# Performance work log

Hardware: AMD Instinct MI355X
Metric: run time of the kernel (lower is better)

Reference implementation:

```python
import jax, jax.numpy as jnp
import numpy as np

R, A, K, N = 4096, 101, 32, 4000000
AEC_LOW, AEC_SPAN = 0.0, 1.0
ETA_NEON, ETA_CHILD, ETA_ADULT = 2.0, 1.5, 1.0
SINK_M = 0.5
FEMALE_SHARE = 0.5
THETA_DEV, PHI_REP, THETA_CYC = 1.0, 1.0, 5.0
RATE_ANN, KAPPA = 0.02, 1.0
WA, RA = 15, 65
INHERIT_CONC, INHERIT_FRAC, BIRTH_ENDOW = 1.0, 0.8, 1.0


def setup_inputs() -> dict:
    key = jax.random.key(0)
    ks = jax.random.split(key, 26)
    dt = 1.0 / 365.0
    pop_age = jax.random.uniform(ks[8], (R, A)) * 1e4
    aging_M = jnp.eye(A) * (1.0 - dt) + jnp.eye(A, A, k=1) * dt
    aging_M = aging_M.at[A - 1, A - 1].set(1.0)
    return {
        'aec_r': jax.random.uniform(ks[0], (R,)) * 2.0,
        'gdp_pc_r': jax.random.uniform(ks[1], (R,)) * 5e4 + 1e3,
        'gdp_pc_ema_R': jax.random.uniform(ks[2], (R,)) * 5e4 + 1e3,
        'gdp_pc_baseline_R': jax.random.uniform(ks[3], (R,)) * 5e4 + 1e3,
        'dev_index_R': jax.random.uniform(ks[4], (R,)),
        'sink_use': jax.random.uniform(ks[5], (R,)),
        'sink_cap': jax.random.uniform(ks[6], (R,)) + 0.5,
        'hazard_A_base': jax.random.uniform(ks[7], (A,)) * 0.1 + 0.001,
        'pop_age': pop_age,
        'population': pop_age.sum(axis=1),
        'aging_M': aging_M,
        'asfr_vector': jax.random.uniform(ks[9], (35,)) * 0.2,
        'distance': jax.random.uniform(ks[10], (R, R)) * 100.0 + 1.0,
        'consump_w_age': jax.random.uniform(ks[11], (A,)),
        'participation_w_age': jax.random.uniform(ks[12], (A,)),
        'consump_base_R': jax.random.uniform(ks[13], (R,)) * 1e4 + 1e3,
        'labor_base_R': jax.random.uniform(ks[14], (R,)) * 1e4 + 1e3,
        'greed': jax.random.uniform(ks[15], (N,)) + 0.01,
        'eATP': jax.random.uniform(ks[16], (N,)) * 100.0,
        'eADP': jax.random.uniform(ks[17], (N,)) * 100.0,
        'eAMP': jax.random.uniform(ks[18], (N,)) * 100.0,
        'pool_atp_R': jax.random.uniform(ks[19], (R,)) * 1e6,
        'pool_adp_R': jax.random.uniform(ks[20], (R,)) * 1e6,
        'pool_amp_R': jax.random.uniform(ks[21], (R,)) * 1e6,
        'nbr_idx': jax.random.randint(ks[22], (R, K), 0, R),
        'agent_region': jax.random.randint(ks[23], (N,), 0, R),
    }


def _forward(aec_r, gdp_pc_r, gdp_pc_ema_R, gdp_pc_baseline_R, dev_index_R, sink_use, sink_cap,
             hazard_A_base, pop_age, population, aging_M, asfr_vector, distance, consump_w_age,
             participation_w_age, consump_base_R, labor_base_R, greed, eATP, eADP, eAMP,
             pool_atp_R, pool_adp_R, pool_amp_R, nbr_idx, agent_region):
    eps = 1e-9
    dt = 1.0 / 365.0
    aec_norm = jnp.clip((aec_r - AEC_LOW) / AEC_SPAN, 0.0, 1.0)
    gdp_prev = gdp_pc_ema_R
    gdp_ema = gdp_prev * 0.9 + 0.1 * gdp_pc_r
    g_ratio = jnp.log(jnp.maximum(gdp_ema / (gdp_pc_baseline_R + eps), 1e-6))
    g_term = jnp.clip(0.5 + 0.5 * jnp.tanh(0.5 * g_ratio), 0.0, 1.0)
    util = jnp.clip(sink_use / (sink_cap + eps), 0.0, 1.0)
    H = jnp.clip(0.5 * aec_norm + 0.4 * g_term + 0.1 * (1.0 - util), 0.0, 1.0)
    dev_proxy = jnp.clip(0.5 + 0.5 * jnp.tanh(0.3 * g_ratio), 0.0, 1.0)
    dev = dev_index_R * 0.99 + 0.01 * dev_proxy
    # age-bucketed hazard multipliers: age 0 / ages 1..14 / ages 15+
    ages = jnp.arange(A)[None, :]
    m_neon = jnp.exp(-ETA_NEON * H)[:, None]
    m_child = jnp.exp(-ETA_CHILD * H)[:, None]
    m_adult = jnp.exp(-ETA_ADULT * H)[:, None]
    mult = jnp.where(ages == 0, m_neon, jnp.where(ages < 15, m_child, m_adult))
    haz = jnp.clip(hazard_A_base[None, :] * mult * (1.0 + SINK_M * util[:, None]), 0.0, 5.0)
    S = jnp.exp(-haz * dt)
    survivors = pop_age * S
    pop_after = survivors @ aging_M  # [R, A]
    deaths_R = jnp.maximum(pop_age.sum(1) - survivors.sum(1), 0.0)
    death_frac_R = jnp.clip(deaths_R / (population + eps), 0.0, 0.99)
    # fertility
    female_RF = FEMALE_SHARE * pop_after[:, 15:50]
    surv_u5 = jnp.exp(-haz[:, 0:5].sum(1))
    F_dev = jnp.clip(jnp.exp(-THETA_DEV * dev), 0.5, 1.5)
    F_rep = jnp.clip((0.995 / jnp.maximum(surv_u5, 1e-3)) ** PHI_REP, 0.5, 1.8)
    g_growth = jnp.log(jnp.maximum(gdp_ema + eps, 1e-6)) - jnp.log(jnp.maximum(gdp_prev + eps, 1e-6))
    F_cyc = jnp.clip(jnp.exp(-THETA_CYC * jnp.maximum(-g_growth, 0.0)), 0.6, 1.2)
    F_total = jnp.clip(F_dev * F_rep * F_cyc, 0.4, 1.8)
    births = jnp.maximum((female_RF * asfr_vector[None, :]).sum(1) * F_total * dt, 0.0)
    births_surv = births * jnp.exp(-haz[:, 0] * dt)
    pop_after = pop_after.at[:, 0].add(births_surv)
    # migration gather-scatter over neighbor regions
    a0, a1 = 18, 40
    mobile = pop_after[:, a0:a1]
    attract = 0.6 * (gdp_pc_r / (gdp_pc_baseline_R + eps)) + 0.4 * (0.5 + 0.5 * aec_norm)
    attract = attract / (attract.mean() + eps)
    dist = jnp.take_along_axis(distance, nbr_idx, axis=1)  # [R, K]
    cost = 1.0 + dist / (dist.mean() + eps)
    w = jax.nn.relu(attract[nbr_idx] / cost ** KAPPA)
    w = w / (w.sum(1, keepdims=True) + eps)
    frac_move = min(max(RATE_ANN * dt, 0.0), 0.25)
    out_R = mobile.sum(1) * frac_move
    move = out_R[:, None] * w  # [R, K]
    age_share = mobile / (mobile.sum(1, keepdims=True) + eps)
    pop_after = pop_after.at[:, a0:a1].add(-age_share * move.sum(1, keepdims=True))
    inflow = (age_share[:, None, :] * move[:, :, None]).reshape(R * K, a1 - a0)
    add = jnp.zeros((R, a1 - a0), pop_after.dtype).at[nbr_idx.reshape(-1)].add(inflow)
    pop_after = pop_after.at[:, a0:a1].add(add)
    pop_new = jnp.maximum(pop_after, 0.0)
    population_new = jnp.maximum(pop_new.sum(1), 0.0)
    consump_scale = jnp.clip((pop_new * consump_w_age[None, :]).sum(1) / (consump_base_R + eps), 0.25, 4.0)
    labor_factor = jnp.clip((pop_new * participation_w_age[None, :]).sum(1) / (labor_base_R + eps), 0.2, 1.2)
    work = pop_new[:, WA:RA].sum(1)
    young = pop_new[:, :WA].sum(1)
    old = pop_new[:, RA:].sum(1)
    psr = work / (old + eps)
    dep = (young + old) / (work + eps)
    # agent-level death / inheritance scatters
    dfi = death_frac_R[agent_region]
    w_raw = (greed + 1e-9) ** INHERIT_CONC
    w_sum_r = jax.ops.segment_sum(w_raw, agent_region, num_segments=R)
    w_norm = w_raw / (w_sum_r[agent_region] + eps)

    def settle(wallet, pool):
        removed = wallet * dfi
        removed_pool = jax.ops.segment_sum(removed, agent_region, num_segments=R)
        heir_pool = removed_pool * INHERIT_FRAC
        wallet2 = wallet - removed + w_norm * heir_pool[agent_region]
        return wallet2, pool - (removed_pool - heir_pool)

    eATP2, pool_atp2 = settle(eATP, pool_atp_R)
    eADP2, pool_adp2 = settle(eADP, pool_adp_R)
    eAMP2, pool_amp2 = settle(eAMP, pool_amp_R)
    counts = jax.ops.segment_sum(jnp.ones_like(dfi), agent_region, num_segments=R)
    eATP2 = eATP2 + BIRTH_ENDOW * (births_surv / jnp.maximum(counts, 1.0))[agent_region]
    return (pop_new, population_new, gdp_ema, dev, H, consump_scale, labor_factor, psr, dep,
            eATP2, eADP2, eAMP2, pool_atp2, pool_adp2, pool_amp2)


def reference(aec_r, gdp_pc_r, gdp_pc_ema_R, gdp_pc_baseline_R, dev_index_R, sink_use, sink_cap,
              hazard_A_base, pop_age, population, aging_M, asfr_vector, distance, consump_w_age,
              participation_w_age, consump_base_R, labor_base_R, greed, eATP, eADP, eAMP,
              pool_atp_R, pool_adp_R, pool_amp_R, nbr_idx, agent_region):
    return _forward(aec_r, gdp_pc_r, gdp_pc_ema_R, gdp_pc_baseline_R, dev_index_R, sink_use,
                    sink_cap, hazard_A_base, pop_age, population, aging_M, asfr_vector, distance,
                    consump_w_age, participation_w_age, consump_base_R, labor_base_R, greed,
                    eATP, eADP, eAMP, pool_atp_R, pool_adp_R, pool_amp_R, nbr_idx, agent_region)
```

## Files before the change

kernel.cpp:

```cpp
#include <hip/hip_runtime.h>

#define RR 4096
#define AA 101
#define PAD_W 104
#define KK 32
#define NAG 4000000

#define NCHUNK 32
#define DR 512
#define NRANGE 8
#define EPB (RR * KK / NCHUNK)
#define CH 8
#define NB 512

static constexpr float EPS  = 1e-9f;
static constexpr float DT   = 1.0f / 365.0f;
static constexpr float FRAC_MOVE = 0.02f / 365.0f;

static constexpr float SC13  = 8192.0f;
static constexpr float INV13 = 1.0f / 8192.0f;
static constexpr float SC20  = 1048576.0f;
static constexpr float INV20 = 1.0f / 1048576.0f;
static constexpr float SC18  = 262144.0f;
static constexpr float INV18 = 1.0f / 262144.0f;

#define OUT_POP   0
#define OUT_POPN  413696
#define OUT_GDP   417792
#define OUT_DEV   421888
#define OUT_H     425984
#define OUT_CONS  430080
#define OUT_LAB   434176
#define OUT_PSR   438272
#define OUT_DEP   442368
#define OUT_ATP   446464
#define OUT_ADP   4446464
#define OUT_AMP   8446464
#define OUT_PATP  12446464
#define OUT_PADP  12450560
#define OUT_PAMP  12454656

static __device__ __forceinline__ float clampf(float x, float lo, float hi) {
    return fminf(fmaxf(x, lo), hi);
}
static __device__ __forceinline__ float wred(float x) {
#pragma unroll
    for (int m = 32; m; m >>= 1) x += __shfl_xor(x, m);
    return x;
}

__global__ __launch_bounds__(256) void k_region1(
    const float* __restrict__ aec, const float* __restrict__ gdp_pc,
    const float* __restrict__ gdp_ema_in, const float* __restrict__ gdp_base,
    const float* __restrict__ dev_in, const float* __restrict__ sink_use,
    const float* __restrict__ sink_cap, const float* __restrict__ haz_base,
    const float* __restrict__ pop_age, const float* __restrict__ population,
    const float* __restrict__ aging, const float* __restrict__ asfr,
    const float* __restrict__ distance, const int* __restrict__ nbr,
    float* __restrict__ Wpa, float* __restrict__ Wdfrac, float* __restrict__ Wbsurv,
    float* __restrict__ Wattr, float* __restrict__ Wgdist, float* __restrict__ Wdsum,
    float* __restrict__ O)
{
    int wid = threadIdx.x >> 6, lane = threadIdx.x & 63;
    int r = blockIdx.x * 4 + wid;

    float aec_norm = clampf(aec[r], 0.0f, 1.0f);
    float gprev = gdp_ema_in[r];
    float gema  = gprev * 0.9f + 0.1f * gdp_pc[r];
    float base  = gdp_base[r];
    float g_ratio = logf(fmaxf(gema / (base + EPS), 1e-6f));
    float g_term  = clampf(0.5f + 0.5f * tanhf(0.5f * g_ratio), 0.0f, 1.0f);
    float util = clampf(sink_use[r] / (sink_cap[r] + EPS), 0.0f, 1.0f);
    float H = clampf(0.5f * aec_norm + 0.4f * g_term + 0.1f * (1.0f - util), 0.0f, 1.0f);
    float dev_proxy = clampf(0.5f + 0.5f * tanhf(0.3f * g_ratio), 0.0f, 1.0f);
    float dev = dev_in[r] * 0.99f + 0.01f * dev_proxy;

    float m_neon  = expf(-2.0f * H);
    float m_child = expf(-1.5f * H);
    float m_adult = expf(-1.0f * H);
    float hazmul = 1.0f + 0.5f * util;

    int a0 = lane * 2, a1 = a0 + 1;
    bool v0 = (a0 < AA), v1 = (a1 < AA);

    float p0 = 0.f, p1 = 0.f, hz0 = 0.f, hz1 = 0.f;
    if (v0) {
        p0 = pop_age[r * AA + a0];
        float mult = (a0 == 0) ? m_neon : ((a0 < 15) ? m_child : m_adult);
        hz0 = clampf(haz_base[a0] * mult * hazmul, 0.0f, 5.0f);
    }
    if (v1) {
        p1 = pop_age[r * AA + a1];
        float mult = (a1 < 15) ? m_child : m_adult;
        hz1 = clampf(haz_base[a1] * mult * hazmul, 0.0f, 5.0f);
    }
    float s0 = v0 ? p0 * expf(-hz0 * DT) : 0.f;
    float s1 = v1 ? p1 * expf(-hz1 * DT) : 0.f;
    float sp = __shfl_up(s1, 1);

    float Md0 = 0.f, Md1 = 0.f, Ms0 = 0.f, Ms1 = 0.f;
    if (v0) { Md0 = aging[a0 * AA + a0]; if (a0 > 0) Ms0 = aging[(a0 - 1) * AA + a0]; }
    if (v1) { Md1 = aging[a1 * AA + a1]; Ms1 = aging[(a1 - 1) * AA + a1]; }

    float pa0 = v0 ? ((a0 == 0) ? s0 * Md0 : s0 * Md0 + sp * Ms0) : 0.f;
    float pa1 = v1 ? (s1 * Md1 + s0 * Ms1) : 0.f;

    if (v0 && a0 > 0) Wpa[r * PAD_W + a0] = pa0;
    if (v1)           Wpa[r * PAD_W + a1] = pa1;

    float pop_sum  = wred(p0 + p1);
    float surv_sum = wred(s0 + s1);
    float haz05 = wred(((v0 && a0 < 5) ? hz0 : 0.f) + ((v1 && a1 < 5) ? hz1 : 0.f));
    float bs0 = (a0 >= 15 && a0 < 50) ? 0.5f * pa0 * asfr[a0 - 15] : 0.f;
    float bs1 = (a1 >= 15 && a1 < 50) ? 0.5f * pa1 * asfr[a1 - 15] : 0.f;
    float b_sum = wred(bs0 + bs1);

    float dc = 0.f;
    if (lane < KK) {
        int idx = nbr[r * KK + lane];
        float d = distance[(size_t)r * RR + idx];
        Wgdist[r * KK + lane] = d;
        dc = d;
    }
    float dsum = wred(dc);

    if (lane == 0) {
        O[OUT_GDP + r] = gema;
        O[OUT_DEV + r] = dev;
        O[OUT_H + r]   = H;

        float deaths = fmaxf(pop_sum - surv_sum, 0.0f);
        Wdfrac[r] = clampf(deaths / (population[r] + EPS), 0.0f, 0.99f);

        float surv_u5 = expf(-haz05);
        float F_dev = clampf(expf(-dev), 0.5f, 1.5f);
        float F_rep = clampf(0.995f / fmaxf(surv_u5, 0.001f), 0.5f, 1.8f);
        float g_growth = logf(fmaxf(gema + EPS, 1e-6f)) - logf(fmaxf(gprev + EPS, 1e-6f));
        float F_cyc = clampf(expf(-5.0f * fmaxf(-g_growth, 0.0f)), 0.6f, 1.2f);
        float F_total = clampf(F_dev * F_rep * F_cyc, 0.4f, 1.8f);
        float births = fmaxf(b_sum * F_total * DT, 0.0f);
        float bsurv = births * expf(-hz0 * DT);
        Wbsurv[r] = bsurv;
        Wpa[r * PAD_W + 0] = pa0 + bsurv;

        Wattr[r] = 0.6f * (gdp_pc[r] / (base + EPS)) + 0.4f * (0.5f + 0.5f * aec_norm);
        Wdsum[r] = dsum;
    }
}

__global__ __launch_bounds__(256) void k_migrate_a(
    const int* __restrict__ nbr, const float* __restrict__ Wattr,
    const float* __restrict__ Wgdist, const float* __restrict__ Wdsum,
    float* __restrict__ Wpa, float* __restrict__ Wash, float* __restrict__ Wmove)
{
    __shared__ float sred[8];
    int t = threadIdx.x;
    {
        float a = 0.f, d = 0.f;
        for (int i = t; i < RR; i += 256) { a += Wattr[i]; d += Wdsum[i]; }
        a = wred(a); d = wred(d);
        int w0 = t >> 6;
        if ((t & 63) == 0) { sred[w0] = a; sred[4 + w0] = d; }
    }
    __syncthreads();
    float asum = sred[0] + sred[1] + sred[2] + sred[3];
    float dall = sred[4] + sred[5] + sred[6] + sred[7];
    float inv_am = 1.0f / (asum / (float)RR + EPS);
    float inv_dm = 1.0f / (dall / (float)(RR * KK) + EPS);

    int wid = t >> 6, lane = t & 63;
    int r = blockIdx.x * 4 + wid;

    float mob = 0.f;
    if (lane < 22) mob = Wpa[r * PAD_W + 18 + lane];
    float msum = wred(lane < 22 ? mob : 0.f);

    float w = 0.f;
    if (lane < KK) {
        int idx = nbr[r * KK + lane];
        float an = Wattr[idx] * inv_am;
        float cost = 1.0f + Wgdist[r * KK + lane] * inv_dm;
        w = fmaxf(an / cost, 0.0f);
    }
    float wsum = wred(lane < KK ? w : 0.f);

    float out_R = msum * FRAC_MOVE;
    float invw = 1.0f / (wsum + EPS);
    float move_sum = out_R * wsum * invw;
    float inv_ms = 1.0f / (msum + EPS);

    if (lane < 22) {
        float ash = mob * inv_ms;
        Wash[r * 22 + lane] = ash;
        Wpa[r * PAD_W + 18 + lane] = mob - ash * move_sum;
    }
    if (lane < KK) Wmove[r * KK + lane] = out_R * w * invw;
}

__global__ __launch_bounds__(256) void k_migrate_b(
    const int* __restrict__ nbr, const float* __restrict__ Wash,
    const float* __restrict__ Wmove, float* __restrict__ Smig)
{
    __shared__ unsigned long long h[11 * DR];
    int range = blockIdx.x & (NRANGE - 1);
    int chunk = blockIdx.x >> 3;
    int d0 = range * DR;

    for (int i = threadIdx.x; i < 11 * DR; i += 256) h[i] = 0ull;
    __syncthreads();

    int tend = (chunk + 1) * EPB;
    for (int t = chunk * EPB + threadIdx.x; t < tend; t += 256) {
        int idx = nbr[t];
        if (idx >= d0 && idx < d0 + DR) {
            int rsrc = t >> 5;
            float mv = Wmove[t];
            const float* ash = &Wash[rsrc * 22];
            int dl = idx - d0;
#pragma unroll
            for (int f = 0; f < 11; f++) {
                unsigned long long lo = __float2uint_rn(ash[2 * f] * mv * SC18);
                unsigned long long hi = __float2uint_rn(ash[2 * f + 1] * mv * SC18);
                atomicAdd(&h[f * DR + dl], lo | (hi << 32));
            }
        }
    }
    __syncthreads();

    for (int i = threadIdx.x; i < 11 * DR; i += 256) {
        int f = i / DR, d = i - f * DR;
        unsigned long long v = h[i];
        Smig[(chunk * 22 + 2 * f) * RR + d0 + d]     = (float)(unsigned int)v * INV18;
        Smig[(chunk * 22 + 2 * f + 1) * RR + d0 + d] = (float)(v >> 32) * INV18;
    }
}

__global__ __launch_bounds__(512, 4) void k_hist(
    const int* __restrict__ reg, const float* __restrict__ greed,
    const float* __restrict__ atp, const float* __restrict__ adp,
    const float* __restrict__ amp, float* __restrict__ S)
{
    __shared__ unsigned long long hAB[RR];
    __shared__ unsigned long long hMGC[RR];
    for (int i = threadIdx.x; i < RR; i += 512) { hAB[i] = 0ull; hMGC[i] = 0ull; }
    __syncthreads();

    const int4*   reg4 = (const int4*)reg;
    const float4* g4 = (const float4*)greed;
    const float4* a4 = (const float4*)atp;
    const float4* d4 = (const float4*)adp;
    const float4* m4 = (const float4*)amp;
    const int NQ = NAG / 4;
    const int STRIDE = NB * 512;

    int q0 = blockIdx.x * 512 + threadIdx.x;
    int4 rrv[4]; float4 gv[4], av[4], dv[4], mv[4];
    bool ok[4];
#pragma unroll
    for (int c = 0; c < 4; c++) {
        int q = q0 + c * STRIDE;
        ok[c] = (q < NQ);
        int qq = ok[c] ? q : 0;
        rrv[c] = reg4[qq];
        gv[c] = g4[qq];
        av[c] = a4[qq];
        dv[c] = d4[qq];
        mv[c] = m4[qq];
    }

#pragma unroll
    for (int c = 0; c < 4; c++) {
        if (!ok[c]) continue;
#define DO1(RX, GX, AX, DX, MX) { \
        unsigned long long ai = __float2uint_rn((AX) * SC13); \
        unsigned long long di = __float2uint_rn((DX) * SC13); \
        unsigned long long mi = __float2uint_rn((MX) * SC13); \
        unsigned long long gi = __float2uint_rn(((GX) + 1e-9f) * SC20); \
        atomicAdd(&hAB[RX],  ai | (di << 32)); \
        atomicAdd(&hMGC[RX], mi | (gi << 28) | (1ull << 56)); }
        DO1(rrv[c].x, gv[c].x, av[c].x, dv[c].x, mv[c].x)
        DO1(rrv[c].y, gv[c].y, av[c].y, dv[c].y, mv[c].y)
        DO1(rrv[c].z, gv[c].z, av[c].z, dv[c].z, mv[c].z)
        DO1(rrv[c].w, gv[c].w, av[c].w, dv[c].w, mv[c].w)
#undef DO1
    }
    __syncthreads();

    int b = blockIdx.x;
    for (int i = threadIdx.x; i < RR; i += 512) {
        unsigned long long ab = hAB[i], mgc = hMGC[i];
        S[((size_t)0 * NB + b) * RR + i] = (float)(unsigned int)ab * INV13;
        S[((size_t)1 * NB + b) * RR + i] = (float)(ab >> 32) * INV13;
        S[((size_t)2 * NB + b) * RR + i] = (float)(mgc & 0xFFFFFFFull) * INV13;
        S[((size_t)3 * NB + b) * RR + i] = (float)((mgc >> 28) & 0xFFFFFFFull) * INV20;
        S[((size_t)4 * NB + b) * RR + i] = (float)(mgc >> 56);
    }
}

__global__ __launch_bounds__(256) void k_reduce(
    const float* __restrict__ S, const float* __restrict__ Smig,
    float* __restrict__ T, float* __restrict__ Wadd)
{
    int blk = blockIdx.x;
    if (blk < 640) {
        int tid = blk * 256 + threadIdx.x;
        int r = tid & (RR - 1);
        int c = (tid >> 12) & (CH - 1);
        int s = tid >> 15;
        int bpc = NB >> 3;
        float acc = 0.f;
        for (int b = c * bpc; b < (c + 1) * bpc; b++)
            acc += S[((size_t)s * NB + b) * RR + r];
        T[(s * CH + c) * RR + r] = acc;
    } else {
        int t2 = (blk - 640) * 256 + threadIdx.x;
        int f = t2 >> 12, rr = t2 & (RR - 1);
        float acc = 0.f;
#pragma unroll
        for (int c = 0; c < NCHUNK; c++)
            acc += Smig[(c * 22 + f) * RR + rr];
        Wadd[rr * 24 + f] = acc;
    }
}

__global__ __launch_bounds__(256) void k_fin(
    const float* __restrict__ Wpa, const float* __restrict__ Wadd,
    const float* __restrict__ cw, const float* __restrict__ pw,
    const float* __restrict__ cbase, const float* __restrict__ lbase,
    const float* __restrict__ T,
    const float* __restrict__ Wdfrac, const float* __restrict__ Wbsurv,
    const float* __restrict__ patp, const float* __restrict__ padp,
    const float* __restrict__ pamp,
    float4* __restrict__ P4, float2* __restrict__ P2,
    float* __restrict__ O)
{
    int blk = blockIdx.x;
    if (blk < 1024) {
        int wid = threadIdx.x >> 6, lane = threadIdx.x & 63;
        int r = blk * 4 + wid;
        int a0 = lane * 2, a1 = a0 + 1;
        bool v0 = (a0 < AA), v1 = (a1 < AA);

        float va = 0.f, vb = 0.f;
        if (lane < 51) {
            float2 pp = *(const float2*)&Wpa[r * PAD_W + a0];
            va = pp.x; vb = pp.y;
        }
        if (a0 >= 18 && a0 < 40) {
            float2 ad = *(const float2*)&Wadd[r * 24 + (a0 - 18)];
            va += ad.x; vb += ad.y;
        }
        va = v0 ? fmaxf(va, 0.0f) : 0.f;
        vb = v1 ? fmaxf(vb, 0.0f) : 0.f;
        if (v0) O[OUT_POP + r * AA + a0] = va;
        if (v1) O[OUT_POP + r * AA + a1] = vb;

        float cw0 = v0 ? cw[a0] : 0.f, cw1 = v1 ? cw[a1] : 0.f;
        float pw0 = v0 ? pw[a0] : 0.f, pw1 = v1 ? pw[a1] : 0.f;

        float psum  = wred(va + vb);
        float cdot  = wred(va * cw0 + vb * cw1);
        float ldot  = wred(va * pw0 + vb * pw1);
        float young = wred(((a0 < 15) ? va : 0.f) + ((a1 < 15) ? vb : 0.f));
        float work  = wred(((a0 >= 15 && a0 < 65) ? va : 0.f) + ((a1 >= 15 && a1 < 65) ? vb : 0.f));
        float old   = wred(((a0 >= 65) ? va : 0.f) + ((a1 >= 65) ? vb : 0.f));

        if (lane == 0) {
            O[OUT_POPN + r] = fmaxf(psum, 0.0f);
            O[OUT_CONS + r] = clampf(cdot / (cbase[r] + EPS), 0.25f, 4.0f);
            O[OUT_LAB + r]  = clampf(ldot / (lbase[r] + EPS), 0.2f, 1.2f);
            O[OUT_PSR + r]  = work / (old + EPS);
            O[OUT_DEP + r]  = (young + old) / (work + EPS);
        }
    } else {
        int r = (blk - 1024) * 256 + threadIdx.x;
        if (r >= RR) return;
        float sums[5];
#pragma unroll
        for (int s = 0; s < 5; s++) {
            float acc = 0.f;
#pragma unroll
            for (int c = 0; c < CH; c++)
                acc += T[(s * CH + c) * RR + r];
            sums[s] = acc;
        }
        float dfi = Wdfrac[r];
        float ra = sums[0] * dfi;
        float rd = sums[1] * dfi;
        float rm = sums[2] * dfi;
        O[OUT_PATP + r] = patp[r] - ra * 0.2f;
        O[OUT_PADP + r] = padp[r] - rd * 0.2f;
        O[OUT_PAMP + r] = pamp[r] - rm * 0.2f;
        P4[r] = make_float4(1.0f - dfi, 1.0f / (sums[3] + EPS), ra * 0.8f, rd * 0.8f);
        P2[r] = make_float2(rm * 0.8f, Wbsurv[r] / fmaxf(sums[4], 1.0f));
    }
}

__global__ __launch_bounds__(256) void k_apply(
    const int* __restrict__ reg, const float* __restrict__ greed,
    const float* __restrict__ atp, const float* __restrict__ adp,
    const float* __restrict__ amp,
    const float4* __restrict__ P4, const float2* __restrict__ P2,
    float* __restrict__ O)
{
    int q = blockIdx.x * 256 + threadIdx.x;
    if (q >= NAG / 4) return;
    int4 rr = ((const int4*)reg)[q];
    float4 g = ((const float4*)greed)[q];
    float4 a = ((const float4*)atp)[q];
    float4 d = ((const float4*)adp)[q];
    float4 m = ((const float4*)amp)[q];
    float4 oa, od, om;
#define ONE(c) { float4 t4 = P4[rr.c]; float2 t2 = P2[rr.c]; \
    float wn = (g.c + 1e-9f) * t4.y; \
    oa.c = a.c * t4.x + wn * t4.z + t2.y; \
    od.c = d.c * t4.x + wn * t4.w; \
    om.c = m.c * t4.x + wn * t2.x; }
    ONE(x) ONE(y) ONE(z) ONE(w)
#undef ONE
    ((float4*)(O + OUT_ATP))[q] = oa;
    ((float4*)(O + OUT_ADP))[q] = od;
    ((float4*)(O + OUT_AMP))[q] = om;
}

extern "C" void kernel_launch(void* const* d_in, const int* in_sizes, int n_in,
                              void* d_out, int out_size, void* d_ws, size_t ws_size,
                              hipStream_t stream) {
    const float* aec       = (const float*)d_in[0];
    const float* gdp_pc    = (const float*)d_in[1];
    const float* gdp_ema   = (const float*)d_in[2];
    const float* gdp_base  = (const float*)d_in[3];
    const float* dev_in    = (const float*)d_in[4];
    const float* sink_use  = (const float*)d_in[5];
    const float* sink_cap  = (const float*)d_in[6];
    const float* haz_base  = (const float*)d_in[7];
    const float* pop_age   = (const float*)d_in[8];
    const float* population= (const float*)d_in[9];
    const float* aging     = (const float*)d_in[10];
    const float* asfr      = (const float*)d_in[11];
    const float* distance  = (const float*)d_in[12];
    const float* cw        = (const float*)d_in[13];
    const float* pw        = (const float*)d_in[14];
    const float* cbase     = (const float*)d_in[15];
    const float* lbase     = (const float*)d_in[16];
    const float* greed     = (const float*)d_in[17];
    const float* eATP      = (const float*)d_in[18];
    const float* eADP      = (const float*)d_in[19];
    const float* eAMP      = (const float*)d_in[20];
    const float* patp      = (const float*)d_in[21];
    const float* padp      = (const float*)d_in[22];
    const float* pamp      = (const float*)d_in[23];
    const int*   nbr       = (const int*)d_in[24];
    const int*   reg       = (const int*)d_in[25];

    float* O = (float*)d_out;

    float* W = (float*)d_ws;
    float* Wpa    = W;
    float* Wdfrac = Wpa    + RR * PAD_W;
    float* Wbsurv = Wdfrac + RR;
    float* Wattr  = Wbsurv + RR;
    float* Wdsum  = Wattr  + RR;
    float* Wgdist = Wdsum  + RR;
    float* Wash   = Wgdist + RR * KK;
    float* Wmove  = Wash   + RR * 22;
    float* P4f    = Wmove  + RR * KK;
    float* P2f    = P4f    + RR * 4;
    float* Wadd   = P2f    + RR * 2;
    float* T      = Wadd   + RR * 24;
    float* Smig   = T      + 5 * CH * RR;
    float* S      = Smig   + (size_t)NCHUNK * 22 * RR;

    k_region1<<<RR / 4, 256, 0, stream>>>(
        aec, gdp_pc, gdp_ema, gdp_base, dev_in, sink_use, sink_cap, haz_base,
        pop_age, population, aging, asfr, distance, nbr,
        Wpa, Wdfrac, Wbsurv, Wattr, Wgdist, Wdsum, O);

    k_migrate_a<<<RR / 4, 256, 0, stream>>>(nbr, Wattr, Wgdist, Wdsum, Wpa, Wash, Wmove);

    k_migrate_b<<<NRANGE * NCHUNK, 256, 0, stream>>>(nbr, Wash, Wmove, Smig);

    k_hist<<<NB, 512, 0, stream>>>(reg, greed, eATP, eADP, eAMP, S);

    k_reduce<<<640 + (22 * RR) / 256, 256, 0, stream>>>(S, Smig, T, Wadd);

    k_fin<<<1024 + RR / 256, 256, 0, stream>>>(
        Wpa, Wadd, cw, pw, cbase, lbase, T, Wdfrac, Wbsurv,
        patp, padp, pamp, (float4*)P4f, (float2*)P2f, O);

    k_apply<<<(NAG / 4 + 255) / 256, 256, 0, stream>>>(
        reg, greed, eATP, eADP, eAMP, (const float4*)P4f, (const float2*)P2f, O);
}
```

Measured before the change: 107.7 us.

## Split histogram kernel into two block groups with one shared histogram each

The per-agent histogram kernel now launches twice as many blocks. Half accumulate the packed ATP/ADP sums and the other half accumulate the packed AMP/greed/count sums, so each block needs only one 32 KB shared array. The smaller shared footprint and the higher launch-bounds occupancy hint are meant to raise occupancy and latency hiding. The cost is that the region index array is read twice, and the register-prefetched unrolled loads become a simple strided loop.

```diff
diff --git a/kernel.cpp b/kernel.cpp
--- a/kernel.cpp
+++ b/kernel.cpp
@@ -235,65 +235,66 @@
     }
 }
 
-__global__ __launch_bounds__(512, 4) void k_hist(
+__global__ __launch_bounds__(512, 8) void k_hist(
     const int* __restrict__ reg, const float* __restrict__ greed,
     const float* __restrict__ atp, const float* __restrict__ adp,
     const float* __restrict__ amp, float* __restrict__ S)
 {
-    __shared__ unsigned long long hAB[RR];
-    __shared__ unsigned long long hMGC[RR];
-    for (int i = threadIdx.x; i < RR; i += 512) { hAB[i] = 0ull; hMGC[i] = 0ull; }
+    __shared__ unsigned long long h[RR];
+    for (int i = threadIdx.x; i < RR; i += 512) h[i] = 0ull;
     __syncthreads();
 
-    const int4*   reg4 = (const int4*)reg;
-    const float4* g4 = (const float4*)greed;
-    const float4* a4 = (const float4*)atp;
-    const float4* d4 = (const float4*)adp;
-    const float4* m4 = (const float4*)amp;
+    const int4* reg4 = (const int4*)reg;
     const int NQ = NAG / 4;
     const int STRIDE = NB * 512;
-
-    int q0 = blockIdx.x * 512 + threadIdx.x;
-    int4 rrv[4]; float4 gv[4], av[4], dv[4], mv[4];
-    bool ok[4];
-#pragma unroll
-    for (int c = 0; c < 4; c++) {
-        int q = q0 + c * STRIDE;
-        ok[c] = (q < NQ);
-        int qq = ok[c] ? q : 0;
-        rrv[c] = reg4[qq];
-        gv[c] = g4[qq];
-        av[c] = a4[qq];
-        dv[c] = d4[qq];
-        mv[c] = m4[qq];
-    }
-
-#pragma unroll
-    for (int c = 0; c < 4; c++) {
-        if (!ok[c]) continue;
-#define DO1(RX, GX, AX, DX, MX) { \
-        unsigned long long ai = __float2uint_rn((AX) * SC13); \
-        unsigned long long di = __float2uint_rn((DX) * SC13); \
-        unsigned long long mi = __float2uint_rn((MX) * SC13); \
-        unsigned long long gi = __float2uint_rn(((GX) + 1e-9f) * SC20); \
-        atomicAdd(&hAB[RX],  ai | (di << 32)); \
-        atomicAdd(&hMGC[RX], mi | (gi << 28) | (1ull << 56)); }
-        DO1(rrv[c].x, gv[c].x, av[c].x, dv[c].x, mv[c].x)
-        DO1(rrv[c].y, gv[c].y, av[c].y, dv[c].y, mv[c].y)
-        DO1(rrv[c].z, gv[c].z, av[c].z, dv[c].z, mv[c].z)
-        DO1(rrv[c].w, gv[c].w, av[c].w, dv[c].w, mv[c].w)
+    int bid = blockIdx.x;
+
+    if (bid < NB) {
+        const float4* a4 = (const float4*)atp;
+        const float4* d4 = (const float4*)adp;
+        for (int q = bid * 512 + threadIdx.x; q < NQ; q += STRIDE) {
+            int4 rr = reg4[q];
+            float4 av = a4[q], dv = d4[q];
+#define DO1(RX, AX, DX) { \
+            unsigned long long ai = __float2uint_rn((AX) * SC13); \
+            unsigned long long di = __float2uint_rn((DX) * SC13); \
+            atomicAdd(&h[RX], ai | (di << 32)); }
+            DO1(rr.x, av.x, dv.x)
+            DO1(rr.y, av.y, dv.y)
+            DO1(rr.z, av.z, dv.z)
+            DO1(rr.w, av.w, dv.w)
 #undef DO1
-    }
-    __syncthreads();
-
-    int b = blockIdx.x;
-    for (int i = threadIdx.x; i < RR; i += 512) {
-        unsigned long long ab = hAB[i], mgc = hMGC[i];
-        S[((size_t)0 * NB + b) * RR + i] = (float)(unsigned int)ab * INV13;
-        S[((size_t)1 * NB + b) * RR + i] = (float)(ab >> 32) * INV13;
-        S[((size_t)2 * NB + b) * RR + i] = (float)(mgc & 0xFFFFFFFull) * INV13;
-        S[((size_t)3 * NB + b) * RR + i] = (float)((mgc >> 28) & 0xFFFFFFFull) * INV20;
-        S[((size_t)4 * NB + b) * RR + i] = (float)(mgc >> 56);
+        }
+        __syncthreads();
+        for (int i = threadIdx.x; i < RR; i += 512) {
+            unsigned long long ab = h[i];
+            S[((size_t)0 * NB + bid) * RR + i] = (float)(unsigned int)ab * INV13;
+            S[((size_t)1 * NB + bid) * RR + i] = (float)(ab >> 32) * INV13;
+        }
+    } else {
+        int b = bid - NB;
+        const float4* m4 = (const float4*)amp;
+        const float4* g4 = (const float4*)greed;
+        for (int q = b * 512 + threadIdx.x; q < NQ; q += STRIDE) {
+            int4 rr = reg4[q];
+            float4 mv = m4[q], gv = g4[q];
+#define DO1(RX, MX, GX) { \
+            unsigned long long mi = __float2uint_rn((MX) * SC13); \
+            unsigned long long gi = __float2uint_rn(((GX) + 1e-9f) * SC20); \
+            atomicAdd(&h[RX], mi | (gi << 28) | (1ull << 56)); }
+            DO1(rr.x, mv.x, gv.x)
+            DO1(rr.y, mv.y, gv.y)
+            DO1(rr.z, mv.z, gv.z)
+            DO1(rr.w, mv.w, gv.w)
+#undef DO1
+        }
+        __syncthreads();
+        for (int i = threadIdx.x; i < RR; i += 512) {
+            unsigned long long mgc = h[i];
+            S[((size_t)2 * NB + b) * RR + i] = (float)(mgc & 0xFFFFFFFull) * INV13;
+            S[((size_t)3 * NB + b) * RR + i] = (float)((mgc >> 28) & 0xFFFFFFFull) * INV20;
+            S[((size_t)4 * NB + b) * RR + i] = (float)(mgc >> 56);
+        }
     }
 }
 
@@ -480,7 +481,7 @@
 
     k_migrate_b<<<NRANGE * NCHUNK, 256, 0, stream>>>(nbr, Wash, Wmove, Smig);
 
-    k_hist<<<NB, 512, 0, stream>>>(reg, greed, eATP, eADP, eAMP, S);
+    k_hist<<<2 * NB, 512, 0, stream>>>(reg, greed, eATP, eADP, eAMP, S);
 
     k_reduce<<<640 + (22 * RR) / 256, 256, 0, stream>>>(S, Smig, T, Wadd);
 
```

Result: no change. 109.0 us (+1.2%).
